# Optimization experiments

Measured on AMD Instinct MI355X. Metric: run time of the kernel, lower is better.

The kernel has to match this reference:

```python
import jax, jax.numpy as jnp
import numpy as np

B, N, DIM, QK_DIM, HEADS, GS, M = 4, 8000, 256, 128, 8, 128, 256


def setup_inputs() -> dict:
    key = jax.random.key(0)
    ks = jax.random.split(key, 8)
    normed_x = jax.random.normal(ks[0], (B, N, DIM), jnp.float32)
    # idx_last is a per-batch permutation (token reordering index), shape [B, N, 1]
    idx_last = jax.vmap(lambda k: jax.random.permutation(k, N))(
        jax.random.split(ks[1], B)).astype(jnp.int32)[..., None]
    k_global = jax.random.normal(ks[2], (HEADS, M, QK_DIM // HEADS), jnp.float32)
    v_global = jax.random.normal(ks[3], (HEADS, M, DIM // HEADS), jnp.float32)
    s = 1.0 / np.sqrt(DIM).astype(np.float32)
    Wq = jax.random.normal(ks[4], (QK_DIM, DIM), jnp.float32) * s
    Wk = jax.random.normal(ks[5], (QK_DIM, DIM), jnp.float32) * s
    Wv = jax.random.normal(ks[6], (DIM, DIM), jnp.float32) * s
    Wp = jax.random.normal(ks[7], (DIM, DIM), jnp.float32) * s
    return {"normed_x": normed_x, "idx_last": idx_last, "k_global": k_global,
            "v_global": v_global, "Wq": Wq, "Wk": Wk, "Wv": Wv, "Wp": Wp}


def _forward(normed_x, idx_last, k_global, v_global, Wq, Wk, Wv, Wp):
    x = normed_x
    b, n, _ = x.shape
    h = HEADS
    idx = idx_last[..., 0]  # [B, N]

    q = x @ Wq.T  # [B, N, QK_DIM]
    k = x @ Wk.T  # [B, N, QK_DIM]
    v = x @ Wv.T  # [B, N, DIM]

    # reorder tokens (gather along the token axis)
    q = jnp.take_along_axis(q, idx[:, :, None], axis=1)
    k = jnp.take_along_axis(k, idx[:, :, None], axis=1)
    v = jnp.take_along_axis(v, idx[:, :, None], axis=1)

    gs = min(n, GS)
    ng = (n + gs - 1) // gs
    pad_n = ng * gs - n

    # pad queries by reflecting the tail, then split into ng groups of gs
    pq = jnp.concatenate([q, jnp.flip(q[:, n - pad_n:n], axis=1)], axis=1)
    pq = pq.reshape(b, ng, gs, h, -1).transpose(0, 1, 3, 2, 4)  # b ng h gs dq

    # keys/values padded with an extra gs of reflected tail -> overlapping windows
    kr = jnp.concatenate([k, jnp.flip(k[:, n - pad_n - gs:n], axis=1)], axis=1)
    vr = jnp.concatenate([v, jnp.flip(v[:, n - pad_n - gs:n], axis=1)], axis=1)
    k_win = jnp.concatenate([kr[:, :ng * gs].reshape(b, ng, gs, -1),
                             kr[:, gs:].reshape(b, ng, gs, -1)], axis=2)
    v_win = jnp.concatenate([vr[:, :ng * gs].reshape(b, ng, gs, -1),
                             vr[:, gs:].reshape(b, ng, gs, -1)], axis=2)
    pk = k_win.reshape(b, ng, 2 * gs, h, -1).transpose(0, 1, 3, 2, 4)  # b ng h 2gs dq
    pv = v_win.reshape(b, ng, 2 * gs, h, -1).transpose(0, 1, 3, 2, 4)  # b ng h 2gs dv

    scale = pq.shape[-1] ** (-0.5)

    # local overlapping-window attention
    s1 = jnp.einsum('bghqd,bghkd->bghqk', pq, pk) * scale
    o1 = jnp.einsum('bghqk,bghkd->bghqd', jax.nn.softmax(s1, axis=-1), pv)

    # global attention (k_global/v_global broadcast over batch and groups)
    s2 = jnp.einsum('bghqd,hmd->bghqm', pq, k_global) * scale
    o2 = jnp.einsum('bghqm,hmd->bghqd', jax.nn.softmax(s2, axis=-1), v_global)

    out = (o1 + o2).transpose(0, 1, 3, 2, 4).reshape(b, ng * gs, -1)[:, :n]

    # scatter back to original token order: res[b, idx[b, i]] = out[b, i]
    b_idx = jnp.arange(b)[:, None]
    out = out.at[b_idx, idx].set(out)
    return out @ Wp.T


def reference(normed_x, idx_last, k_global, v_global, Wq, Wk, Wv, Wp):
    return _forward(normed_x, idx_last, k_global, v_global, Wq, Wk, Wv, Wp)
```

## Files before the change

### kernel.cpp

```cpp
#include <hip/hip_runtime.h>

typedef __attribute__((ext_vector_type(8))) short short8;
typedef __attribute__((ext_vector_type(4))) short short4v;
typedef __attribute__((ext_vector_type(4))) float f32x4;
typedef unsigned short ushort_t;

#define MFMA_BF16_K32(A,B,C) __builtin_amdgcn_mfma_f32_16x16x32_bf16(A,B,C,0,0,0)
#define MFMA_BF16_K16(A,B,C) __builtin_amdgcn_mfma_f32_16x16x16bf16_1k(A,B,C,0,0,0)

static constexpr int Bc  = 4;
static constexpr int Nn  = 8000;
static constexpr int N2  = 8192;
static constexpr int DIMc = 256;
static constexpr float SC2 = 0.36067376022224085f;

__device__ __forceinline__ unsigned short f2bf(float f){
  unsigned int u = __float_as_uint(f);
  u = (u + 0x7FFFu + ((u >> 16) & 1u)) >> 16;
  return (unsigned short)u;
}
__device__ __forceinline__ uint2 pack4(f32x4 v){
  uint2 r;
  r.x = (unsigned)f2bf(v[0]) | ((unsigned)f2bf(v[1]) << 16);
  r.y = (unsigned)f2bf(v[2]) | ((unsigned)f2bf(v[3]) << 16);
  return r;
}
__device__ __forceinline__ unsigned cvtpk(float lo, float hi){
  unsigned r;
  asm("v_cvt_pk_bf16_f32 %0, %1, %2" : "=v"(r) : "v"(lo), "v"(hi));
  return r;
}
__device__ __forceinline__ float rexp2(float x){
  float r;
  asm("v_exp_f32 %0, %1" : "=v"(r) : "v"(x));
  return r;
}
__device__ __forceinline__ int vperm(int t){
  return (t & ~31) | (((t >> 2) & 3) * 8 + ((t >> 4) & 1) * 4 + (t & 3));
}

__global__ __launch_bounds__(256) void prep_kernel(
    const float* __restrict__ Wq, const float* __restrict__ Wk,
    const float* __restrict__ Wv, const float* __restrict__ Wp,
    const float* __restrict__ kg, const float* __restrict__ vg,
    ushort_t* __restrict__ Wcs, ushort_t* __restrict__ Wps,
    ushort_t* __restrict__ vgT, ushort_t* __restrict__ kgb)
{
  int i = blockIdx.x * 256 + threadIdx.x;
  if (i < 131072){
    int jj = i & 7, f = i >> 3;
    int l = f & 63, kc = (f >> 6) & 7, ctw = f >> 9;
    int col = ctw * 16 + (l & 15);
    int k   = kc * 32 + (l >> 4) * 8 + jj;
    float v;
    if (col < 128)      v = Wq[col * 256 + k] * SC2;
    else if (col < 256) v = Wk[(col - 128) * 256 + k];
    else                v = Wv[(col - 256) * 256 + k];
    Wcs[i] = f2bf(v);
  } else if (i < 196608){
    int o = i - 131072;
    int jj = o & 7, f = o >> 3;
    int l = f & 63, kc = (f >> 6) & 7, ctw = f >> 9;
    int col = ctw * 16 + (l & 15);
    int k   = kc * 32 + (l >> 4) * 8 + jj;
    Wps[o] = f2bf(Wp[col * 256 + k]);
  } else if (i < 262144){
    int o = i - 196608;
    int c = o & 31, m = (o >> 5) & 255, h = o >> 13;
    vgT[(h * 32 + c) * 256 + vperm(m)] = f2bf(vg[o]);
  } else {
    int j = i - 262144;
    kgb[j] = f2bf(kg[j]);
  }
}

__global__ __launch_bounds__(256) void proj_kernel(
    const float* __restrict__ X, const ushort_t* __restrict__ Wcs,
    const int* __restrict__ idx, ushort_t* __restrict__ qh,
    ushort_t* __restrict__ kh, ushort_t* __restrict__ vT)
{
  const int b  = blockIdx.y;
  const int r0 = blockIdx.x * 64;
  const int tid = threadIdx.x;
  const int w = tid >> 6, l = tid & 63, g4 = l >> 4, q16 = l & 15;
  __shared__ unsigned Xs[64][132];

  #pragma unroll
  for (int r = 0; r < 16; ++r){
    int row = r * 4 + w;
    int tok = idx[b * Nn + r0 + row];
    float4 xv = reinterpret_cast<const float4*>(X + (size_t)(b * Nn + tok) * DIMc)[l];
    uint2 u; u.x = cvtpk(xv.x, xv.y); u.y = cvtpk(xv.z, xv.w);
    *reinterpret_cast<uint2*>(&Xs[row][l * 2]) = u;
  }
  __syncthreads();

  f32x4 acc[4][8];
  #pragma unroll
  for (int mt = 0; mt < 4; ++mt)
    #pragma unroll
    for (int ct = 0; ct < 8; ++ct) acc[mt][ct] = f32x4{0.f, 0.f, 0.f, 0.f};
  #pragma unroll
  for (int kc = 0; kc < 8; ++kc){
    short8 a[4];
    #pragma unroll
    for (int mt = 0; mt < 4; ++mt){
      uint4 au = *reinterpret_cast<const uint4*>(&Xs[mt * 16 + q16][kc * 16 + g4 * 4]);
      a[mt] = __builtin_bit_cast(short8, au);
    }
    #pragma unroll
    for (int ct = 0; ct < 8; ++ct){
      short8 bb = *reinterpret_cast<const short8*>(
          Wcs + ((size_t)((w * 8 + ct) * 8 + kc) * 64 + l) * 8);
      #pragma unroll
      for (int mt = 0; mt < 4; ++mt) acc[mt][ct] = MFMA_BF16_K32(a[mt], bb, acc[mt][ct]);
    }
  }
  if (w < 2){
    ushort_t* dst = (w == 0) ? qh : kh;
    #pragma unroll
    for (int ct = 0; ct < 8; ++ct){
      #pragma unroll
      for (int mt = 0; mt < 4; ++mt){
        #pragma unroll
        for (int r = 0; r < 4; ++r){
          int j = r0 + mt * 16 + g4 * 4 + r;
          dst[((size_t)(b * 8 + ct) * N2 + j) * 16 + q16] = f2bf(acc[mt][ct][r]);
        }
      }
    }
  } else {
    #pragma unroll
    for (int ct = 0; ct < 8; ++ct){
      int col = (w - 2) * 128 + ct * 16 + q16;
      #pragma unroll
      for (int mt = 0; mt < 4; ++mt){
        int jb = r0 + (mt >> 1) * 32 + g4 * 8 + (mt & 1) * 4;
        *reinterpret_cast<uint2*>(vT + (size_t)(b * 256 + col) * N2 + jb) = pack4(acc[mt][ct]);
      }
    }
  }
}

__global__ __launch_bounds__(256) void reflect_fill_kernel(
    ushort_t* __restrict__ qh, ushort_t* __restrict__ kh, ushort_t* __restrict__ vT)
{
  int t = blockIdx.x * 256 + threadIdx.x;
  if (t < 24576){
    int e = t & 1;
    int r = (t >> 1) % 192;
    int p = (t >> 1) / 192;
    int b = p >> 4, q = p & 15;
    ushort_t* base = (q < 8) ? qh : kh;
    int h = q & 7;
    size_t plane = (size_t)(b * 8 + h) * N2 * 16;
    const uint4* src = reinterpret_cast<const uint4*>(base + plane + (size_t)(7999 - r) * 16);
    uint4*       dst = reinterpret_cast<uint4*>(base + plane + (size_t)(8000 + r) * 16);
    dst[e] = src[e];
  } else {
    int u = t - 24576;
    int r = u / 192, i2 = u % 192;
    vT[(size_t)r * N2 + vperm(8000 + i2)] = vT[(size_t)r * N2 + vperm(7999 - i2)];
  }
}

__global__ __launch_bounds__(256) void attn_kernel(
    const ushort_t* __restrict__ qh, const ushort_t* __restrict__ kh,
    const ushort_t* __restrict__ vT,
    const ushort_t* __restrict__ kg, const ushort_t* __restrict__ vgT,
    ushort_t* __restrict__ aoh0, ushort_t* __restrict__ aoh1)
{
  const int go = blockIdx.x, hp = blockIdx.y, b = blockIdx.z;
  const int tid = threadIdx.x;
  const int w = tid >> 6, l = tid & 63, g4 = l >> 4, q16 = l & 15;
  const int h = hp * 2 + (w >> 1);
  const int pass = w & 1;
  const f32x4 z4 = {0.f, 0.f, 0.f, 0.f};
  const size_t bh = (size_t)(b * 8 + h);
  const ushort_t* Qb = qh + (bh * N2 + go * 128) * 16;
  ushort_t*       Ob = (pass ? aoh1 : aoh0) + (bh * N2 + go * 128) * 32;

  short8 ones;
  #pragma unroll
  for (int j = 0; j < 8; ++j) ones[j] = (short)0x3F80;

  const ushort_t* kbase = pass ? (kg + (size_t)h * 256 * 16)
                               : (kh + (bh * N2 + go * 128) * 16);
  short4v karr[16];
  #pragma unroll
  for (int t = 0; t < 16; ++t)
    karr[t] = *reinterpret_cast<const short4v*>(
        kbase + (size_t)(t * 16 + q16) * 16 + g4 * 4);
  const ushort_t* v0;
  size_t rstride;
  if (!pass){
    v0 = vT + (size_t)(b * 256 + h * 32) * N2 + go * 128 + (size_t)q16 * N2 + g4 * 8;
    rstride = (size_t)16 * N2;
  } else {
    v0 = vgT + (size_t)h * 32 * 256 + (size_t)q16 * 256 + g4 * 8;
    rstride = (size_t)16 * 256;
  }
  uint4 va[8], vb[8];
  #pragma unroll
  for (int t2 = 0; t2 < 8; ++t2){
    va[t2] = *reinterpret_cast<const uint4*>(v0 + t2 * 32);
    vb[t2] = *reinterpret_cast<const uint4*>(v0 + rstride + t2 * 32);
  }

  #pragma unroll 2
  for (int qt = 0; qt < 8; ++qt){
    short4v qf = *reinterpret_cast<const short4v*>(
        Qb + (size_t)(qt * 16 + q16) * 16 + g4 * 4);
    f32x4 s[16];
    __builtin_amdgcn_s_setprio(1);
    #pragma unroll
    for (int t = 0; t < 16; ++t) s[t] = MFMA_BF16_K16(karr[t], qf, z4);
    __builtin_amdgcn_s_setprio(0);
    uint4 p4[8];
    #pragma unroll
    for (int t2 = 0; t2 < 8; ++t2){
      float e0 = rexp2(s[2*t2][0]);
      float e1 = rexp2(s[2*t2][1]);
      float e2 = rexp2(s[2*t2][2]);
      float e3 = rexp2(s[2*t2][3]);
      float f0 = rexp2(s[2*t2+1][0]);
      float f1 = rexp2(s[2*t2+1][1]);
      float f2 = rexp2(s[2*t2+1][2]);
      float f3 = rexp2(s[2*t2+1][3]);
      p4[t2].x = cvtpk(e0, e1); p4[t2].y = cvtpk(e2, e3);
      p4[t2].z = cvtpk(f0, f1); p4[t2].w = cvtpk(f2, f3);
    }
    f32x4 o0 = z4, o1 = z4, dacc = z4;
    __builtin_amdgcn_s_setprio(1);
    #pragma unroll
    for (int t2 = 0; t2 < 8; ++t2){
      short8 pf = __builtin_bit_cast(short8, p4[t2]);
      o0   = MFMA_BF16_K32(__builtin_bit_cast(short8, va[t2]), pf, o0);
      o1   = MFMA_BF16_K32(__builtin_bit_cast(short8, vb[t2]), pf, o1);
      dacc = MFMA_BF16_K32(ones, pf, dacc);
    }
    __builtin_amdgcn_s_setprio(0);
    float invd = 1.0f / dacc[0];
    uint2 s0, s1;
    s0.x = cvtpk(o0[0] * invd, o0[1] * invd);
    s0.y = cvtpk(o0[2] * invd, o0[3] * invd);
    s1.x = cvtpk(o1[0] * invd, o1[1] * invd);
    s1.y = cvtpk(o1[2] * invd, o1[3] * invd);
    size_t base = (size_t)(qt * 16 + q16) * 32;
    *reinterpret_cast<uint2*>(Ob + base + g4 * 4)      = s0;
    *reinterpret_cast<uint2*>(Ob + base + 16 + g4 * 4) = s1;
  }
}

__global__ __launch_bounds__(256) void final_kernel(
    const ushort_t* __restrict__ A0, const ushort_t* __restrict__ A1,
    const ushort_t* __restrict__ Wps,
    const int* __restrict__ idx, float* __restrict__ out)
{
  const int b  = blockIdx.y;
  const int r0 = blockIdx.x * 64;
  const int tid = threadIdx.x;
  const int w = tid >> 6, l = tid & 63, g4 = l >> 4, q16 = l & 15;
  f32x4 acc[4][4];
  #pragma unroll
  for (int mt = 0; mt < 4; ++mt)
    #pragma unroll
    for (int ct = 0; ct < 4; ++ct) acc[mt][ct] = f32x4{0.f, 0.f, 0.f, 0.f};
  #pragma unroll
  for (int kc = 0; kc < 8; ++kc){
    short8 a0[4], a1[4];
    #pragma unroll
    for (int mt = 0; mt < 4; ++mt){
      size_t off = ((size_t)(b * 8 + kc) * N2 + r0 + mt * 16 + q16) * 32 + g4 * 8;
      a0[mt] = *reinterpret_cast<const short8*>(A0 + off);
      a1[mt] = *reinterpret_cast<const short8*>(A1 + off);
    }
    #pragma unroll
    for (int ct = 0; ct < 4; ++ct){
      short8 bb = *reinterpret_cast<const short8*>(
          Wps + ((size_t)((w * 4 + ct) * 8 + kc) * 64 + l) * 8);
      #pragma unroll
      for (int mt = 0; mt < 4; ++mt){
        acc[mt][ct] = MFMA_BF16_K32(a0[mt], bb, acc[mt][ct]);
        acc[mt][ct] = MFMA_BF16_K32(a1[mt], bb, acc[mt][ct]);
      }
    }
  }
  #pragma unroll
  for (int mt = 0; mt < 4; ++mt){
    int orow[4];
    #pragma unroll
    for (int r = 0; r < 4; ++r) orow[r] = idx[b * Nn + r0 + mt * 16 + g4 * 4 + r];
    #pragma unroll
    for (int ct = 0; ct < 4; ++ct){
      int col = w * 64 + ct * 16 + q16;
      #pragma unroll
      for (int r = 0; r < 4; ++r)
        out[(size_t)(b * Nn + orow[r]) * DIMc + col] = acc[mt][ct][r];
    }
  }
}

extern "C" void kernel_launch(void* const* d_in, const int* in_sizes, int n_in,
                              void* d_out, int out_size, void* d_ws, size_t ws_size,
                              hipStream_t stream)
{
  const float* x   = (const float*)d_in[0];
  const int*   idx = (const int*)d_in[1];
  const float* kg  = (const float*)d_in[2];
  const float* vg  = (const float*)d_in[3];
  const float* Wq  = (const float*)d_in[4];
  const float* Wk  = (const float*)d_in[5];
  const float* Wv  = (const float*)d_in[6];
  const float* Wp  = (const float*)d_in[7];
  float* out = (float*)d_out;

  char* ws = (char*)d_ws;
  size_t off = 0;
  auto alloc = [&](size_t bytes) -> void* {
    void* p = ws + off; off += (bytes + 255) & ~(size_t)255; return p;
  };
  ushort_t* qh   = (ushort_t*)alloc((size_t)Bc * 8 * N2 * 16 * 2);
  ushort_t* kh   = (ushort_t*)alloc((size_t)Bc * 8 * N2 * 16 * 2);
  ushort_t* vT   = (ushort_t*)alloc((size_t)Bc * 256 * N2 * 2);
  ushort_t* aoh0 = (ushort_t*)alloc((size_t)Bc * 8 * N2 * 32 * 2);
  ushort_t* aoh1 = (ushort_t*)alloc((size_t)Bc * 8 * N2 * 32 * 2);
  ushort_t* Wcs  = (ushort_t*)alloc((size_t)512 * 256 * 2);
  ushort_t* Wps  = (ushort_t*)alloc((size_t)256 * 256 * 2);
  ushort_t* vgT  = (ushort_t*)alloc((size_t)8 * 32 * 256 * 2);
  ushort_t* kgb  = (ushort_t*)alloc((size_t)8 * 256 * 16 * 2);

  hipLaunchKernelGGL(prep_kernel,  dim3(1152), dim3(256), 0, stream,
                     Wq, Wk, Wv, Wp, kg, vg, Wcs, Wps, vgT, kgb);
  hipLaunchKernelGGL(proj_kernel,  dim3(125, 4), dim3(256), 0, stream, x, Wcs, idx, qh, kh, vT);
  hipLaunchKernelGGL(reflect_fill_kernel, dim3(864), dim3(256), 0, stream, qh, kh, vT);
  hipLaunchKernelGGL(attn_kernel,  dim3(63, 4, 4), dim3(256), 0, stream,
                     qh, kh, vT, kgb, vgT, aoh0, aoh1);
  hipLaunchKernelGGL(final_kernel, dim3(125, 4), dim3(256), 0, stream, aoh0, aoh1, Wps, idx, out);
}
```

Measured before the change: 95.66 us.

## Fuse attention and output projection into one kernel via LDS staging

Merges the attention kernel and the final projection/scatter kernel. Each 1024-thread block now handles all 8 heads and both passes for a 128-token group. It writes the bf16 attention outputs into padded shared memory and then runs the Wp GEMM and scatter directly. This removes the global round trip of two large intermediate buffers and one kernel launch. In exchange the grid shrinks from 1008 to 252 blocks with large LDS use per block, which may reduce occupancy and parallelism.

```diff
diff --git a/kernel.cpp b/kernel.cpp
--- a/kernel.cpp
+++ b/kernel.cpp
@@ -12,6 +12,7 @@
 static constexpr int Nn  = 8000;
 static constexpr int N2  = 8192;
 static constexpr int DIMc = 256;
+static constexpr int AP  = 520;
 static constexpr float SC2 = 0.36067376022224085f;
 
 __device__ __forceinline__ unsigned short f2bf(float f){
@@ -164,21 +165,21 @@
   }
 }
 
-__global__ __launch_bounds__(256) void attn_kernel(
+__global__ __launch_bounds__(1024) void attn_final_kernel(
     const ushort_t* __restrict__ qh, const ushort_t* __restrict__ kh,
     const ushort_t* __restrict__ vT,
     const ushort_t* __restrict__ kg, const ushort_t* __restrict__ vgT,
-    ushort_t* __restrict__ aoh0, ushort_t* __restrict__ aoh1)
-{
-  const int go = blockIdx.x, hp = blockIdx.y, b = blockIdx.z;
+    const ushort_t* __restrict__ Wps,
+    const int* __restrict__ idx, float* __restrict__ out)
+{
+  extern __shared__ ushort_t Asm[];
+  const int go = blockIdx.x, b = blockIdx.y;
   const int tid = threadIdx.x;
-  const int w = tid >> 6, l = tid & 63, g4 = l >> 4, q16 = l & 15;
-  const int h = hp * 2 + (w >> 1);
-  const int pass = w & 1;
+  const int wv = tid >> 6, l = tid & 63, g4 = l >> 4, q16 = l & 15;
+  const int h = wv >> 1, pass = wv & 1;
   const f32x4 z4 = {0.f, 0.f, 0.f, 0.f};
   const size_t bh = (size_t)(b * 8 + h);
   const ushort_t* Qb = qh + (bh * N2 + go * 128) * 16;
-  ushort_t*       Ob = (pass ? aoh1 : aoh0) + (bh * N2 + go * 128) * 32;
 
   short8 ones;
   #pragma unroll
@@ -246,57 +247,48 @@
     s0.y = cvtpk(o0[2] * invd, o0[3] * invd);
     s1.x = cvtpk(o1[0] * invd, o1[1] * invd);
     s1.y = cvtpk(o1[2] * invd, o1[3] * invd);
-    size_t base = (size_t)(qt * 16 + q16) * 32;
-    *reinterpret_cast<uint2*>(Ob + base + g4 * 4)      = s0;
-    *reinterpret_cast<uint2*>(Ob + base + 16 + g4 * 4) = s1;
-  }
-}
-
-__global__ __launch_bounds__(256) void final_kernel(
-    const ushort_t* __restrict__ A0, const ushort_t* __restrict__ A1,
-    const ushort_t* __restrict__ Wps,
-    const int* __restrict__ idx, float* __restrict__ out)
-{
-  const int b  = blockIdx.y;
-  const int r0 = blockIdx.x * 64;
-  const int tid = threadIdx.x;
-  const int w = tid >> 6, l = tid & 63, g4 = l >> 4, q16 = l & 15;
-  f32x4 acc[4][4];
-  #pragma unroll
-  for (int mt = 0; mt < 4; ++mt)
+    size_t lbase = (size_t)(qt * 16 + q16) * AP + pass * 256 + h * 32;
+    *reinterpret_cast<uint2*>(&Asm[lbase + g4 * 4])      = s0;
+    *reinterpret_cast<uint2*>(&Asm[lbase + 16 + g4 * 4]) = s1;
+  }
+
+  __syncthreads();
+  const int mw = wv >> 2, cw = wv & 3;
+  f32x4 acc[2][4];
+  #pragma unroll
+  for (int mt = 0; mt < 2; ++mt)
     #pragma unroll
     for (int ct = 0; ct < 4; ++ct) acc[mt][ct] = f32x4{0.f, 0.f, 0.f, 0.f};
   #pragma unroll
-  for (int kc = 0; kc < 8; ++kc){
-    short8 a0[4], a1[4];
-    #pragma unroll
-    for (int mt = 0; mt < 4; ++mt){
-      size_t off = ((size_t)(b * 8 + kc) * N2 + r0 + mt * 16 + q16) * 32 + g4 * 8;
-      a0[mt] = *reinterpret_cast<const short8*>(A0 + off);
-      a1[mt] = *reinterpret_cast<const short8*>(A1 + off);
+  for (int kc = 0; kc < 16; ++kc){
+    short8 a[2];
+    #pragma unroll
+    for (int mt = 0; mt < 2; ++mt){
+      int row = mw * 32 + mt * 16 + q16;
+      a[mt] = *reinterpret_cast<const short8*>(&Asm[(size_t)row * AP + kc * 32 + g4 * 8]);
     }
     #pragma unroll
     for (int ct = 0; ct < 4; ++ct){
       short8 bb = *reinterpret_cast<const short8*>(
-          Wps + ((size_t)((w * 4 + ct) * 8 + kc) * 64 + l) * 8);
-      #pragma unroll
-      for (int mt = 0; mt < 4; ++mt){
-        acc[mt][ct] = MFMA_BF16_K32(a0[mt], bb, acc[mt][ct]);
-        acc[mt][ct] = MFMA_BF16_K32(a1[mt], bb, acc[mt][ct]);
-      }
-    }
-  }
-  #pragma unroll
-  for (int mt = 0; mt < 4; ++mt){
+          Wps + ((size_t)((cw * 4 + ct) * 8 + (kc & 7)) * 64 + l) * 8);
+      #pragma unroll
+      for (int mt = 0; mt < 2; ++mt) acc[mt][ct] = MFMA_BF16_K32(a[mt], bb, acc[mt][ct]);
+    }
+  }
+  #pragma unroll
+  for (int mt = 0; mt < 2; ++mt){
+    int jb = go * 128 + mw * 32 + mt * 16 + g4 * 4;
     int orow[4];
     #pragma unroll
-    for (int r = 0; r < 4; ++r) orow[r] = idx[b * Nn + r0 + mt * 16 + g4 * 4 + r];
+    for (int r = 0; r < 4; ++r)
+      orow[r] = (jb + r < Nn) ? idx[b * Nn + jb + r] : 0;
     #pragma unroll
     for (int ct = 0; ct < 4; ++ct){
-      int col = w * 64 + ct * 16 + q16;
+      int col = cw * 64 + ct * 16 + q16;
       #pragma unroll
       for (int r = 0; r < 4; ++r)
-        out[(size_t)(b * Nn + orow[r]) * DIMc + col] = acc[mt][ct][r];
+        if (jb + r < Nn)
+          out[(size_t)(b * Nn + orow[r]) * DIMc + col] = acc[mt][ct][r];
     }
   }
 }
@@ -323,18 +315,19 @@
   ushort_t* qh   = (ushort_t*)alloc((size_t)Bc * 8 * N2 * 16 * 2);
   ushort_t* kh   = (ushort_t*)alloc((size_t)Bc * 8 * N2 * 16 * 2);
   ushort_t* vT   = (ushort_t*)alloc((size_t)Bc * 256 * N2 * 2);
-  ushort_t* aoh0 = (ushort_t*)alloc((size_t)Bc * 8 * N2 * 32 * 2);
-  ushort_t* aoh1 = (ushort_t*)alloc((size_t)Bc * 8 * N2 * 32 * 2);
   ushort_t* Wcs  = (ushort_t*)alloc((size_t)512 * 256 * 2);
   ushort_t* Wps  = (ushort_t*)alloc((size_t)256 * 256 * 2);
   ushort_t* vgT  = (ushort_t*)alloc((size_t)8 * 32 * 256 * 2);
   ushort_t* kgb  = (ushort_t*)alloc((size_t)8 * 256 * 16 * 2);
 
+  const int lds_bytes = 128 * AP * 2;
+  hipFuncSetAttribute(reinterpret_cast<const void*>(attn_final_kernel),
+                      hipFuncAttributeMaxDynamicSharedMemorySize, lds_bytes);
+
   hipLaunchKernelGGL(prep_kernel,  dim3(1152), dim3(256), 0, stream,
                      Wq, Wk, Wv, Wp, kg, vg, Wcs, Wps, vgT, kgb);
   hipLaunchKernelGGL(proj_kernel,  dim3(125, 4), dim3(256), 0, stream, x, Wcs, idx, qh, kh, vT);
   hipLaunchKernelGGL(reflect_fill_kernel, dim3(864), dim3(256), 0, stream, qh, kh, vT);
-  hipLaunchKernelGGL(attn_kernel,  dim3(63, 4, 4), dim3(256), 0, stream,
-                     qh, kh, vT, kgb, vgT, aoh0, aoh1);
-  hipLaunchKernelGGL(final_kernel, dim3(125, 4), dim3(256), 0, stream, aoh0, aoh1, Wps, idx, out);
-}
+  hipLaunchKernelGGL(attn_final_kernel, dim3(63, 4), dim3(1024), lds_bytes, stream,
+                     qh, kh, vT, kgb, vgT, Wps, idx, out);
+}
```

Result: slower. 150.2 us (+57.0%).
